# Kernel tuning notes

Hardware: AMD Instinct MI355X
Metric: run time of the kernel (lower is better)

Reference implementation:

```python
import jax, jax.numpy as jnp
import numpy as np

N_NODES = 100000
N_EDGES = 1600000
D_IN, D_H, D_OUT = 512, 128, 64
BN_EPS = 1e-5


def setup_inputs() -> dict:
    key = jax.random.key(0)
    ks = jax.random.split(key, 8)
    x = jax.random.normal(ks[0], (N_NODES, D_IN), dtype=jnp.float32)
    # COO sparse normalized adjacency
    row = jnp.sort(jax.random.randint(ks[1], (N_EDGES,), 0, N_NODES))
    col = jax.random.randint(ks[2], (N_EDGES,), 0, N_NODES)
    adj_vals = jax.random.uniform(ks[3], (N_EDGES,), dtype=jnp.float32) / 16.0
    # GraphConvolution params (xavier_uniform weight, zero bias)
    lim0 = float(np.sqrt(6.0 / (D_IN + D_H)))
    lim1 = float(np.sqrt(6.0 / (D_H + D_OUT)))
    W0 = jax.random.uniform(ks[4], (D_IN, D_H), minval=-lim0, maxval=lim0, dtype=jnp.float32)
    W1 = jax.random.uniform(ks[5], (D_H, D_OUT), minval=-lim1, maxval=lim1, dtype=jnp.float32)
    b0 = jnp.zeros((D_H,), dtype=jnp.float32)
    b1 = jnp.zeros((D_OUT,), dtype=jnp.float32)
    return {"x": x, "W0": W0, "b0": b0, "W1": W1, "b1": b1,
            "adj_vals": adj_vals, "row": row, "col": col}


def _spmm(vals, row, col, h, n):
    # (sparse adj) @ h : gather source rows, scale by edge value, scatter-add to dest
    return jax.ops.segment_sum(vals[:, None] * h[col], row, num_segments=n)


def reference(x, W0, b0, W1, b1, adj_vals, row, col):
    n = x.shape[0]
    # layer 0: adj @ (x @ W0) + b0  (dropout is identity in eval mode)
    h = _spmm(adj_vals, row, col, x @ W0, n) + b0
    h = jax.nn.relu(h)
    # BatchNorm1d(affine=False, track_running_stats=False): batch stats, biased var
    mean = jnp.mean(h, axis=0)
    var = jnp.mean(jnp.square(h - mean), axis=0)
    h = (h - mean) * jax.lax.rsqrt(var + BN_EPS)
    # layer 1: adj @ (h @ W1) + b1
    return _spmm(adj_vals, row, col, h @ W1, n) + b1
```

## Files before the change

### kernel.cpp

```cpp
#include <hip/hip_runtime.h>
#include <hip/hip_bf16.h>
#include <cstdint>
#include <cstddef>

#define D_IN  512
#define D_H   128
#define D_OUT 64
#define SB    256

typedef __attribute__((ext_vector_type(8))) short bf16x8;
typedef __attribute__((ext_vector_type(4))) float f32x4;

__device__ __forceinline__ float bf2f(unsigned short u) {
  union { unsigned int i; float f; } v; v.i = ((unsigned int)u) << 16; return v.f;
}
__device__ __forceinline__ unsigned short f2bf(float f) {
  union { unsigned int i; float f; } v; v.f = f;
  unsigned int r = v.i + 0x7FFFu + ((v.i >> 16) & 1u);
  return (unsigned short)(r >> 16);
}
__device__ __forceinline__ unsigned int pk_bf16(float a, float b) {
  union { __hip_bfloat162 h; unsigned int u; } cv;
  cv.h = __float22bfloat162_rn(make_float2(a, b));
  return cv.u;
}

#define OFF_RP    0u
#define OFF_W0T   400384u
#define OFF_W1TP  531456u
#define OFF_CVEC  547840u
#define OFF_PSUM  548096u
#define OFF_PSQ   679168u
#define OFF_H     810240u
#define END_H     26410240u
#define END_HW    39210240u

__global__ void k_init(const int* __restrict__ row, int* __restrict__ rp,
                       const float* __restrict__ W0, unsigned short* __restrict__ W0t,
                       int n, int e, int RB) {
  int b = blockIdx.x, t = threadIdx.x;
  if (b < RB) {
    int i = b * 256 + t;
    if (i > n) return;
    int lo = 0, hi = e;
    while (lo < hi) { int mid = (lo + hi) >> 1; if (row[mid] < i) lo = mid + 1; else hi = mid; }
    rp[i] = lo;
  } else {
    int idx = (b - RB) * 256 + t;
    int k = idx & (D_IN - 1);
    int nn = idx >> 9;
    W0t[nn * D_IN + k] = f2bf(W0[k * D_H + nn]);
  }
}

__global__ __launch_bounds__(256) void k_gemm1(const float* __restrict__ A,
                                               const unsigned short* __restrict__ Bt,
                                               unsigned short* __restrict__ C, int M) {
  __shared__ unsigned short Ash[2][4096];
  __shared__ unsigned short Bsh[2][4096];
  const int tid = threadIdx.x, lane = tid & 63, wave = tid >> 6;
  const int wm = (wave >> 1) * 64, wn = (wave & 1) * 64;
  const int m0 = blockIdx.x * 128, quad = lane >> 4, l16 = lane & 15;
  f32x4 acc[4][4] = {};
  int am[2], ak[2];
  const float* aptr[2];
  const unsigned short* bptr[2];
#pragma unroll
  for (int i = 0; i < 2; ++i) {
    int c = tid + i * 256;
    am[i] = c >> 2; ak[i] = c & 3;
    int gm = m0 + am[i]; if (gm >= M) gm = M - 1;
    aptr[i] = A + (size_t)gm * D_IN + ak[i] * 8;
    bptr[i] = Bt + (size_t)am[i] * D_IN + ak[i] * 8;
  }
  f32x4 areg[2][2]; bf16x8 breg[2];
#pragma unroll
  for (int i = 0; i < 2; ++i) {
    areg[i][0] = *(const f32x4*)(aptr[i]);
    areg[i][1] = *(const f32x4*)(aptr[i] + 4);
    breg[i]    = *(const bf16x8*)(bptr[i]);
  }
  const int NIT = D_IN / 32;
  for (int it = 0; it < NIT; ++it) {
    const int buf = it & 1;
    unsigned short* ash = Ash[buf];
    unsigned short* bsh = Bsh[buf];
#pragma unroll
    for (int i = 0; i < 2; ++i) {
      unsigned int pk4[4];
      pk4[0] = pk_bf16(areg[i][0][0], areg[i][0][1]);
      pk4[1] = pk_bf16(areg[i][0][2], areg[i][0][3]);
      pk4[2] = pk_bf16(areg[i][1][0], areg[i][1][1]);
      pk4[3] = pk_bf16(areg[i][1][2], areg[i][1][3]);
      *(uint4*)&ash[(ak[i] * 128 + am[i]) * 8] = *(uint4*)pk4;
      *(bf16x8*)&bsh[(ak[i] * 128 + am[i]) * 8] = breg[i];
    }
    __syncthreads();
    if (it + 1 < NIT) {
      int k0 = (it + 1) * 32;
#pragma unroll
      for (int i = 0; i < 2; ++i) {
        areg[i][0] = *(const f32x4*)(aptr[i] + k0);
        areg[i][1] = *(const f32x4*)(aptr[i] + k0 + 4);
        breg[i]    = *(const bf16x8*)(bptr[i] + k0);
      }
    }
    bf16x8 af[4], bfv[4];
#pragma unroll
    for (int mf = 0; mf < 4; ++mf)
      af[mf] = *(const bf16x8*)&ash[(quad * 128 + (wm + mf * 16 + l16)) * 8];
#pragma unroll
    for (int nf = 0; nf < 4; ++nf)
      bfv[nf] = *(const bf16x8*)&bsh[(quad * 128 + (wn + nf * 16 + l16)) * 8];
#pragma unroll
    for (int mf = 0; mf < 4; ++mf)
#pragma unroll
      for (int nf = 0; nf < 4; ++nf)
        acc[mf][nf] = __builtin_amdgcn_mfma_f32_16x16x32_bf16(af[mf], bfv[nf], acc[mf][nf], 0, 0, 0);
  }
#pragma unroll
  for (int mf = 0; mf < 4; ++mf)
#pragma unroll
    for (int nf = 0; nf < 4; ++nf)
#pragma unroll
      for (int i = 0; i < 4; ++i) {
        int r = m0 + wm + mf * 16 + quad * 4 + i;
        int cc = wn + nf * 16 + l16;
        if (r < M) C[(size_t)r * D_H + cc] = f2bf(acc[mf][nf][i]);
      }
}

#define ACCP(P, W) { \
  union { unsigned int u; float f; } _t; \
  _t.u = (P).x << 16;         a0 += (W) * _t.f; \
  _t.u = (P).x & 0xFFFF0000u; a1 += (W) * _t.f; \
  _t.u = (P).y << 16;         a2 += (W) * _t.f; \
  _t.u = (P).y & 0xFFFF0000u; a3 += (W) * _t.f; \
  _t.u = (P).z << 16;         a4 += (W) * _t.f; \
  _t.u = (P).z & 0xFFFF0000u; a5 += (W) * _t.f; \
  _t.u = (P).w << 16;         a6 += (W) * _t.f; \
  _t.u = (P).w & 0xFFFF0000u; a7 += (W) * _t.f; }

__global__ __launch_bounds__(256) void k_spmm1(const unsigned int* __restrict__ xw2,
                                               const float* __restrict__ adj,
                                               const int* __restrict__ col,
                                               const int* __restrict__ rp,
                                               const float* __restrict__ b0,
                                               unsigned int* __restrict__ h2, int n) {
  int node = blockIdx.x * 4 + (threadIdx.x >> 6);
  if (node >= n) return;
  const int l = threadIdx.x & 63;
  const int q = l >> 4, s = l & 15;
  const int e0 = rp[node], e1 = rp[node + 1];
  float a0 = 0.f, a1 = 0.f, a2 = 0.f, a3 = 0.f;
  float a4 = 0.f, a5 = 0.f, a6 = 0.f, a7 = 0.f;
  int e = e0;
  for (; e + 16 <= e1; e += 16) {
    int eb = e + 4 * q;
    int   c0 = col[eb],     c1 = col[eb + 1], c2 = col[eb + 2], c3 = col[eb + 3];
    float w0 = adj[eb],     w1 = adj[eb + 1], w2 = adj[eb + 2], w3 = adj[eb + 3];
    uint4 p0 = *(const uint4*)(xw2 + (size_t)c0 * 64 + 4 * s);
    uint4 p1 = *(const uint4*)(xw2 + (size_t)c1 * 64 + 4 * s);
    uint4 p2 = *(const uint4*)(xw2 + (size_t)c2 * 64 + 4 * s);
    uint4 p3 = *(const uint4*)(xw2 + (size_t)c3 * 64 + 4 * s);
    ACCP(p0, w0); ACCP(p1, w1); ACCP(p2, w2); ACCP(p3, w3);
  }
  for (; e < e1; e += 4) {
    int idx = e + q;
    int ic = idx < e1 ? idx : e1 - 1;
    int   c = col[ic];
    float w = idx < e1 ? adj[ic] : 0.f;
    uint4 p = *(const uint4*)(xw2 + (size_t)c * 64 + 4 * s);
    ACCP(p, w);
  }
#define RED2(v) { v += __shfl_xor(v, 16, 64); v += __shfl_xor(v, 32, 64); }
  RED2(a0) RED2(a1) RED2(a2) RED2(a3) RED2(a4) RED2(a5) RED2(a6) RED2(a7)
#undef RED2
  if (q == 0) {
    float4 bl = *(const float4*)(b0 + 8 * s);
    float4 bh = *(const float4*)(b0 + 8 * s + 4);
    float r0 = fmaxf(a0 + bl.x, 0.f), r1 = fmaxf(a1 + bl.y, 0.f);
    float r2 = fmaxf(a2 + bl.z, 0.f), r3 = fmaxf(a3 + bl.w, 0.f);
    float r4 = fmaxf(a4 + bh.x, 0.f), r5 = fmaxf(a5 + bh.y, 0.f);
    float r6 = fmaxf(a6 + bh.z, 0.f), r7 = fmaxf(a7 + bh.w, 0.f);
    uint4 o;
    o.x = ((unsigned int)f2bf(r1) << 16) | (unsigned int)f2bf(r0);
    o.y = ((unsigned int)f2bf(r3) << 16) | (unsigned int)f2bf(r2);
    o.z = ((unsigned int)f2bf(r5) << 16) | (unsigned int)f2bf(r4);
    o.w = ((unsigned int)f2bf(r7) << 16) | (unsigned int)f2bf(r6);
    *(uint4*)(h2 + (size_t)node * 64 + 4 * s) = o;
  }
}

__global__ __launch_bounds__(256) void k_stats(const unsigned int* __restrict__ h2,
                                               float* __restrict__ psum,
                                               float* __restrict__ psq, int n) {
  __shared__ float sA[256], sB[256], qA[256], qB[256];
  int t = threadIdx.x;
  int f2 = t & 63, rg = t >> 6;
  float s0 = 0.f, s1 = 0.f, q0 = 0.f, q1 = 0.f;
  for (int r = blockIdx.x * 4 + rg; r < n; r += gridDim.x * 4) {
    unsigned int p = h2[(size_t)r * 64 + f2];
    float v0 = bf2f((unsigned short)(p & 0xFFFF));
    float v1 = bf2f((unsigned short)(p >> 16));
    s0 += v0; s1 += v1; q0 += v0 * v0; q1 += v1 * v1;
  }
  sA[t] = s0; sB[t] = s1; qA[t] = q0; qB[t] = q1;
  __syncthreads();
  if (t < 64) {
    float S0 = sA[t] + sA[t + 64] + sA[t + 128] + sA[t + 192];
    float S1 = sB[t] + sB[t + 64] + sB[t + 128] + sB[t + 192];
    float Q0 = qA[t] + qA[t + 64] + qA[t + 128] + qA[t + 192];
    float Q1 = qB[t] + qB[t + 64] + qB[t + 128] + qB[t + 192];
    psum[blockIdx.x * 128 + 2 * t]     = S0;
    psum[blockIdx.x * 128 + 2 * t + 1] = S1;
    psq [blockIdx.x * 128 + 2 * t]     = Q0;
    psq [blockIdx.x * 128 + 2 * t + 1] = Q1;
  }
}

__global__ void k_prep2(const float* __restrict__ psum, const float* __restrict__ psq,
                        const float* __restrict__ W1,
                        unsigned short* __restrict__ W1tp, float* __restrict__ cvec, int n) {
  __shared__ float rs[256], rq[256];
  __shared__ float mean_s[128], istd_s[128];
  __shared__ float cpart[256];
  int t = threadIdx.x;
  int f = t & 127, half = t >> 7;
  {
    float s = 0.f, q = 0.f;
#pragma unroll 8
    for (int b = half * (SB / 2); b < (half + 1) * (SB / 2); ++b) {
      s += psum[b * 128 + f]; q += psq[b * 128 + f];
    }
    rs[t] = s; rq[t] = q;
  }
  __syncthreads();
  if (t < 128) {
    float s = rs[t] + rs[t + 128];
    float q = rq[t] + rq[t + 128];
    float m = s / (float)n;
    float var = q / (float)n - m * m;
    if (var < 0.f) var = 0.f;
    mean_s[t] = m;
    istd_s[t] = rsqrtf(var + 1e-5f);
  }
  __syncthreads();
  for (int idx = t; idx < D_OUT * D_H; idx += 256) {
    int nn = idx >> 7, k = idx & 127;
    W1tp[nn * D_H + k] = f2bf(istd_s[k] * W1[k * D_OUT + nn]);
  }
  {
    int o = t & 63, part = t >> 6;
    float a = 0.f;
    for (int k = part * 32; k < part * 32 + 32; ++k)
      a += mean_s[k] * istd_s[k] * W1[k * D_OUT + o];
    cpart[t] = a;
  }
  __syncthreads();
  if (t < D_OUT)
    cvec[t] = -(cpart[t] + cpart[t + 64] + cpart[t + 128] + cpart[t + 192]);
}

__global__ __launch_bounds__(256) void k_gemm2(const unsigned short* __restrict__ A,
                                               const unsigned short* __restrict__ Bt,
                                               const float* __restrict__ cvec,
                                               unsigned short* __restrict__ Cout, int M) {
  __shared__ unsigned short Ash[4096];
  __shared__ unsigned short Bsh[2048];
  const int tid = threadIdx.x, lane = tid & 63, wave = tid >> 6;
  const int wm = wave * 32, m0 = blockIdx.x * 128;
  const int quad = lane >> 4, l16 = lane & 15;
  f32x4 acc[2][4] = {};
  for (int k0 = 0; k0 < D_H; k0 += 32) {
    __syncthreads();
#pragma unroll
    for (int i = 0; i < 2; ++i) {
      int c = tid + i * 256;
      int m = c >> 2, k8 = c & 3;
      int gm = m0 + m; if (gm >= M) gm = M - 1;
      *(bf16x8*)&Ash[(k8 * 128 + m) * 8] = *(const bf16x8*)&A[(size_t)gm * D_H + k0 + k8 * 8];
    }
    {
      int nn = tid >> 2, k8 = tid & 3;
      *(bf16x8*)&Bsh[(k8 * 64 + nn) * 8] = *(const bf16x8*)&Bt[(size_t)nn * D_H + k0 + k8 * 8];
    }
    __syncthreads();
    bf16x8 af[2], bfv[4];
#pragma unroll
    for (int mf = 0; mf < 2; ++mf)
      af[mf] = *(const bf16x8*)&Ash[(quad * 128 + (wm + mf * 16 + l16)) * 8];
#pragma unroll
    for (int nf = 0; nf < 4; ++nf)
      bfv[nf] = *(const bf16x8*)&Bsh[(quad * 64 + (nf * 16 + l16)) * 8];
#pragma unroll
    for (int mf = 0; mf < 2; ++mf)
#pragma unroll
      for (int nf = 0; nf < 4; ++nf)
        acc[mf][nf] = __builtin_amdgcn_mfma_f32_16x16x32_bf16(af[mf], bfv[nf], acc[mf][nf], 0, 0, 0);
  }
#pragma unroll
  for (int mf = 0; mf < 2; ++mf)
#pragma unroll
    for (int nf = 0; nf < 4; ++nf)
#pragma unroll
      for (int i = 0; i < 4; ++i) {
        int r = m0 + wm + mf * 16 + quad * 4 + i;
        int cc = nf * 16 + l16;
        if (r < M) Cout[(size_t)r * 64 + cc] = f2bf(acc[mf][nf][i] + cvec[cc]);
      }
}

__global__ __launch_bounds__(256) void k_spmm2(const unsigned int* __restrict__ hw2,
                                               const float* __restrict__ adj,
                                               const int* __restrict__ col,
                                               const int* __restrict__ rp,
                                               const float* __restrict__ b1,
                                               float* __restrict__ outp, int n) {
  int node = blockIdx.x * 4 + (threadIdx.x >> 6);
  if (node >= n) return;
  const int l = threadIdx.x & 63;
  const int g = l >> 3, s = l & 7;
  const int e0 = rp[node], e1 = rp[node + 1];
  float a0 = 0.f, a1 = 0.f, a2 = 0.f, a3 = 0.f;
  float a4 = 0.f, a5 = 0.f, a6 = 0.f, a7 = 0.f;
  int e = e0;
  for (; e + 16 <= e1; e += 16) {
    int eb = e + 2 * g;
    int   c0 = col[eb],  c1 = col[eb + 1];
    float w0 = adj[eb],  w1 = adj[eb + 1];
    uint4 p0 = *(const uint4*)(hw2 + (size_t)c0 * 32 + 4 * s);
    uint4 p1 = *(const uint4*)(hw2 + (size_t)c1 * 32 + 4 * s);
    ACCP(p0, w0); ACCP(p1, w1);
  }
  for (; e < e1; e += 8) {
    int idx = e + g;
    int ic = idx < e1 ? idx : e1 - 1;
    int   c = col[ic];
    float w = idx < e1 ? adj[ic] : 0.f;
    uint4 p = *(const uint4*)(hw2 + (size_t)c * 32 + 4 * s);
    ACCP(p, w);
  }
#define RED3(v) { v += __shfl_xor(v, 8, 64); v += __shfl_xor(v, 16, 64); v += __shfl_xor(v, 32, 64); }
  RED3(a0) RED3(a1) RED3(a2) RED3(a3) RED3(a4) RED3(a5) RED3(a6) RED3(a7)
#undef RED3
  if (g == 0) {
    float4 bl = *(const float4*)(b1 + 8 * s);
    float4 bh = *(const float4*)(b1 + 8 * s + 4);
    float4 r0, r1;
    r0.x = a0 + bl.x; r0.y = a1 + bl.y; r0.z = a2 + bl.z; r0.w = a3 + bl.w;
    r1.x = a4 + bh.x; r1.y = a5 + bh.y; r1.z = a6 + bh.z; r1.w = a7 + bh.w;
    *(float4*)(outp + (size_t)node * 64 + 8 * s)     = r0;
    *(float4*)(outp + (size_t)node * 64 + 8 * s + 4) = r1;
  }
}

extern "C" void kernel_launch(void* const* d_in, const int* in_sizes, int n_in,
                              void* d_out, int out_size, void* d_ws, size_t ws_size,
                              hipStream_t stream) {
  const float* x   = (const float*)d_in[0];
  const float* W0  = (const float*)d_in[1];
  const float* b0  = (const float*)d_in[2];
  const float* W1  = (const float*)d_in[3];
  const float* b1  = (const float*)d_in[4];
  const float* adj = (const float*)d_in[5];
  const int* row = (const int*)d_in[6];
  const int* col = (const int*)d_in[7];
  const int N = in_sizes[0] / D_IN;
  const int E = in_sizes[5];

  char* ws = (char*)d_ws;
  int*            rp   = (int*)(ws + OFF_RP);
  unsigned short* W0t  = (unsigned short*)(ws + OFF_W0T);
  unsigned short* W1tp = (unsigned short*)(ws + OFF_W1TP);
  float*          cvec = (float*)(ws + OFF_CVEC);
  float*          psum = (float*)(ws + OFF_PSUM);
  float*          psq  = (float*)(ws + OFF_PSQ);
  unsigned short* h    = (unsigned short*)(ws + OFF_H);

  unsigned short* xw = (unsigned short*)d_out;
  const bool hw_in_ws = (ws_size >= (size_t)END_HW);
  unsigned short* hwp  = hw_in_ws ? (unsigned short*)(ws + END_H) : (unsigned short*)d_out;
  float*          outd = hw_in_ws ? (float*)d_out                 : (float*)(ws + OFF_H);

  const int RB = (N + 1 + 255) / 256;
  const int TB = (D_IN * D_H) / 256;
  k_init<<<RB + TB, 256, 0, stream>>>(row, rp, W0, W0t, N, E, RB);
  k_gemm1<<<(N + 127) / 128, 256, 0, stream>>>(x, W0t, xw, N);
  k_spmm1<<<(N + 3) / 4, 256, 0, stream>>>((const unsigned int*)xw, adj, col, rp, b0,
                                           (unsigned int*)h, N);
  k_stats<<<SB, 256, 0, stream>>>((const unsigned int*)h, psum, psq, N);
  k_prep2<<<1, 256, 0, stream>>>(psum, psq, W1, W1tp, cvec, N);
  k_gemm2<<<(N + 127) / 128, 256, 0, stream>>>(h, W1tp, cvec, hwp, N);
  k_spmm2<<<(N + 3) / 4, 256, 0, stream>>>((const unsigned int*)hwp, adj, col, rp, b1,
                                           outd, N);
  if (!hw_in_ws) {
    hipMemcpyAsync(d_out, outd, (size_t)N * D_OUT * sizeof(float),
                   hipMemcpyDeviceToDevice, stream);
  }
}
```

Measured before the change: 491.9 us.

## Fuse batch-norm statistics into first SpMM via atomic partial sums

The separate statistics kernel, which re-read the whole hidden activation buffer, is removed. Each SpMM1 block now reduces its four rows' sums and squared sums in shared memory and atomically adds them into one of 64 zero-initialised slots. The slots are cleared by an extra block in the init kernel. The intermediate XW buffer moves into the workspace when it is large enough, and the device-to-device copy fallback is dropped. The trade is extra global atomics with contention on 64 slots against one fewer full pass over memory and one fewer launch. Statistics are now taken from fp32 values rather than bf16-rounded ones.

New measurement: 465.6 us. -5.4%, faster.

```diff
diff --git a/kernel.cpp b/kernel.cpp
--- a/kernel.cpp
+++ b/kernel.cpp
@@ -6,7 +6,7 @@
 #define D_IN  512
 #define D_H   128
 #define D_OUT 64
-#define SB    256
+#define SB    64
 
 typedef __attribute__((ext_vector_type(8))) short bf16x8;
 typedef __attribute__((ext_vector_type(4))) float f32x4;
@@ -34,10 +34,13 @@
 #define OFF_H     810240u
 #define END_H     26410240u
 #define END_HW    39210240u
+#define OFF_XW    39210240u
+#define END_XW    64810240u
 
 __global__ void k_init(const int* __restrict__ row, int* __restrict__ rp,
                        const float* __restrict__ W0, unsigned short* __restrict__ W0t,
-                       int n, int e, int RB) {
+                       float* __restrict__ psum, float* __restrict__ psq,
+                       int n, int e, int RB, int TB) {
   int b = blockIdx.x, t = threadIdx.x;
   if (b < RB) {
     int i = b * 256 + t;
@@ -45,11 +48,13 @@
     int lo = 0, hi = e;
     while (lo < hi) { int mid = (lo + hi) >> 1; if (row[mid] < i) lo = mid + 1; else hi = mid; }
     rp[i] = lo;
-  } else {
+  } else if (b < RB + TB) {
     int idx = (b - RB) * 256 + t;
     int k = idx & (D_IN - 1);
     int nn = idx >> 9;
     W0t[nn * D_IN + k] = f2bf(W0[k * D_H + nn]);
+  } else {
+    for (int i = t; i < SB * 128; i += 256) { psum[i] = 0.f; psq[i] = 0.f; }
   }
 }
 
@@ -146,76 +151,70 @@
                                                const int* __restrict__ col,
                                                const int* __restrict__ rp,
                                                const float* __restrict__ b0,
-                                               unsigned int* __restrict__ h2, int n) {
-  int node = blockIdx.x * 4 + (threadIdx.x >> 6);
-  if (node >= n) return;
-  const int l = threadIdx.x & 63;
-  const int q = l >> 4, s = l & 15;
-  const int e0 = rp[node], e1 = rp[node + 1];
-  float a0 = 0.f, a1 = 0.f, a2 = 0.f, a3 = 0.f;
-  float a4 = 0.f, a5 = 0.f, a6 = 0.f, a7 = 0.f;
-  int e = e0;
-  for (; e + 16 <= e1; e += 16) {
-    int eb = e + 4 * q;
-    int   c0 = col[eb],     c1 = col[eb + 1], c2 = col[eb + 2], c3 = col[eb + 3];
-    float w0 = adj[eb],     w1 = adj[eb + 1], w2 = adj[eb + 2], w3 = adj[eb + 3];
-    uint4 p0 = *(const uint4*)(xw2 + (size_t)c0 * 64 + 4 * s);
-    uint4 p1 = *(const uint4*)(xw2 + (size_t)c1 * 64 + 4 * s);
-    uint4 p2 = *(const uint4*)(xw2 + (size_t)c2 * 64 + 4 * s);
-    uint4 p3 = *(const uint4*)(xw2 + (size_t)c3 * 64 + 4 * s);
-    ACCP(p0, w0); ACCP(p1, w1); ACCP(p2, w2); ACCP(p3, w3);
-  }
-  for (; e < e1; e += 4) {
-    int idx = e + q;
-    int ic = idx < e1 ? idx : e1 - 1;
-    int   c = col[ic];
-    float w = idx < e1 ? adj[ic] : 0.f;
-    uint4 p = *(const uint4*)(xw2 + (size_t)c * 64 + 4 * s);
-    ACCP(p, w);
-  }
-#define RED2(v) { v += __shfl_xor(v, 16, 64); v += __shfl_xor(v, 32, 64); }
-  RED2(a0) RED2(a1) RED2(a2) RED2(a3) RED2(a4) RED2(a5) RED2(a6) RED2(a7)
-#undef RED2
-  if (q == 0) {
-    float4 bl = *(const float4*)(b0 + 8 * s);
-    float4 bh = *(const float4*)(b0 + 8 * s + 4);
-    float r0 = fmaxf(a0 + bl.x, 0.f), r1 = fmaxf(a1 + bl.y, 0.f);
-    float r2 = fmaxf(a2 + bl.z, 0.f), r3 = fmaxf(a3 + bl.w, 0.f);
-    float r4 = fmaxf(a4 + bh.x, 0.f), r5 = fmaxf(a5 + bh.y, 0.f);
-    float r6 = fmaxf(a6 + bh.z, 0.f), r7 = fmaxf(a7 + bh.w, 0.f);
-    uint4 o;
-    o.x = ((unsigned int)f2bf(r1) << 16) | (unsigned int)f2bf(r0);
-    o.y = ((unsigned int)f2bf(r3) << 16) | (unsigned int)f2bf(r2);
-    o.z = ((unsigned int)f2bf(r5) << 16) | (unsigned int)f2bf(r4);
-    o.w = ((unsigned int)f2bf(r7) << 16) | (unsigned int)f2bf(r6);
-    *(uint4*)(h2 + (size_t)node * 64 + 4 * s) = o;
-  }
-}
-
-__global__ __launch_bounds__(256) void k_stats(const unsigned int* __restrict__ h2,
+                                               unsigned int* __restrict__ h2,
                                                float* __restrict__ psum,
                                                float* __restrict__ psq, int n) {
-  __shared__ float sA[256], sB[256], qA[256], qB[256];
-  int t = threadIdx.x;
-  int f2 = t & 63, rg = t >> 6;
-  float s0 = 0.f, s1 = 0.f, q0 = 0.f, q1 = 0.f;
-  for (int r = blockIdx.x * 4 + rg; r < n; r += gridDim.x * 4) {
-    unsigned int p = h2[(size_t)r * 64 + f2];
-    float v0 = bf2f((unsigned short)(p & 0xFFFF));
-    float v1 = bf2f((unsigned short)(p >> 16));
-    s0 += v0; s1 += v1; q0 += v0 * v0; q1 += v1 * v1;
-  }
-  sA[t] = s0; sB[t] = s1; qA[t] = q0; qB[t] = q1;
+  __shared__ float sst[512], sqt[512];
+  const int t = threadIdx.x;
+  const int wave = t >> 6, l = t & 63;
+  sst[wave * 128 + l] = 0.f; sst[wave * 128 + 64 + l] = 0.f;
+  sqt[wave * 128 + l] = 0.f; sqt[wave * 128 + 64 + l] = 0.f;
+  const int node = blockIdx.x * 4 + wave;
+  const int q = l >> 4, s = l & 15;
+  if (node < n) {
+    const int e0 = rp[node], e1 = rp[node + 1];
+    float a0 = 0.f, a1 = 0.f, a2 = 0.f, a3 = 0.f;
+    float a4 = 0.f, a5 = 0.f, a6 = 0.f, a7 = 0.f;
+    int e = e0;
+    for (; e + 16 <= e1; e += 16) {
+      int eb = e + 4 * q;
+      int   c0 = col[eb],     c1 = col[eb + 1], c2 = col[eb + 2], c3 = col[eb + 3];
+      float w0 = adj[eb],     w1 = adj[eb + 1], w2 = adj[eb + 2], w3 = adj[eb + 3];
+      uint4 p0 = *(const uint4*)(xw2 + (size_t)c0 * 64 + 4 * s);
+      uint4 p1 = *(const uint4*)(xw2 + (size_t)c1 * 64 + 4 * s);
+      uint4 p2 = *(const uint4*)(xw2 + (size_t)c2 * 64 + 4 * s);
+      uint4 p3 = *(const uint4*)(xw2 + (size_t)c3 * 64 + 4 * s);
+      ACCP(p0, w0); ACCP(p1, w1); ACCP(p2, w2); ACCP(p3, w3);
+    }
+    for (; e < e1; e += 4) {
+      int idx = e + q;
+      int ic = idx < e1 ? idx : e1 - 1;
+      int   c = col[ic];
+      float w = idx < e1 ? adj[ic] : 0.f;
+      uint4 p = *(const uint4*)(xw2 + (size_t)c * 64 + 4 * s);
+      ACCP(p, w);
+    }
+#define RED2(v) { v += __shfl_xor(v, 16, 64); v += __shfl_xor(v, 32, 64); }
+    RED2(a0) RED2(a1) RED2(a2) RED2(a3) RED2(a4) RED2(a5) RED2(a6) RED2(a7)
+#undef RED2
+    if (q == 0) {
+      float4 bl = *(const float4*)(b0 + 8 * s);
+      float4 bh = *(const float4*)(b0 + 8 * s + 4);
+      float r0 = fmaxf(a0 + bl.x, 0.f), r1 = fmaxf(a1 + bl.y, 0.f);
+      float r2 = fmaxf(a2 + bl.z, 0.f), r3 = fmaxf(a3 + bl.w, 0.f);
+      float r4 = fmaxf(a4 + bh.x, 0.f), r5 = fmaxf(a5 + bh.y, 0.f);
+      float r6 = fmaxf(a6 + bh.z, 0.f), r7 = fmaxf(a7 + bh.w, 0.f);
+      uint4 o;
+      o.x = ((unsigned int)f2bf(r1) << 16) | (unsigned int)f2bf(r0);
+      o.y = ((unsigned int)f2bf(r3) << 16) | (unsigned int)f2bf(r2);
+      o.z = ((unsigned int)f2bf(r5) << 16) | (unsigned int)f2bf(r4);
+      o.w = ((unsigned int)f2bf(r7) << 16) | (unsigned int)f2bf(r6);
+      *(uint4*)(h2 + (size_t)node * 64 + 4 * s) = o;
+      float* sw = sst + wave * 128 + 8 * s;
+      float* qw = sqt + wave * 128 + 8 * s;
+      sw[0] = r0; sw[1] = r1; sw[2] = r2; sw[3] = r3;
+      sw[4] = r4; sw[5] = r5; sw[6] = r6; sw[7] = r7;
+      qw[0] = r0 * r0; qw[1] = r1 * r1; qw[2] = r2 * r2; qw[3] = r3 * r3;
+      qw[4] = r4 * r4; qw[5] = r5 * r5; qw[6] = r6 * r6; qw[7] = r7 * r7;
+    }
+  }
   __syncthreads();
-  if (t < 64) {
-    float S0 = sA[t] + sA[t + 64] + sA[t + 128] + sA[t + 192];
-    float S1 = sB[t] + sB[t + 64] + sB[t + 128] + sB[t + 192];
-    float Q0 = qA[t] + qA[t + 64] + qA[t + 128] + qA[t + 192];
-    float Q1 = qB[t] + qB[t + 64] + qB[t + 128] + qB[t + 192];
-    psum[blockIdx.x * 128 + 2 * t]     = S0;
-    psum[blockIdx.x * 128 + 2 * t + 1] = S1;
-    psq [blockIdx.x * 128 + 2 * t]     = Q0;
-    psq [blockIdx.x * 128 + 2 * t + 1] = Q1;
+  if (t < 128) {
+    float S = sst[t] + sst[128 + t] + sst[256 + t] + sst[384 + t];
+    float Q = sqt[t] + sqt[128 + t] + sqt[256 + t] + sqt[384 + t];
+    int slot = (blockIdx.x & (SB - 1)) * 128 + t;
+    atomicAdd(&psum[slot], S);
+    atomicAdd(&psq[slot], Q);
   }
 }
 
@@ -378,24 +377,19 @@
   float*          psq  = (float*)(ws + OFF_PSQ);
   unsigned short* h    = (unsigned short*)(ws + OFF_H);
 
-  unsigned short* xw = (unsigned short*)d_out;
-  const bool hw_in_ws = (ws_size >= (size_t)END_HW);
-  unsigned short* hwp  = hw_in_ws ? (unsigned short*)(ws + END_H) : (unsigned short*)d_out;
-  float*          outd = hw_in_ws ? (float*)d_out                 : (float*)(ws + OFF_H);
+  const bool big_ws = (ws_size >= (size_t)END_XW);
+  unsigned short* xw   = big_ws ? (unsigned short*)(ws + OFF_XW) : (unsigned short*)d_out;
+  unsigned short* hwp  = big_ws ? (unsigned short*)(ws + END_H)  : (unsigned short*)d_out;
+  float*          outd = (float*)d_out;
 
   const int RB = (N + 1 + 255) / 256;
   const int TB = (D_IN * D_H) / 256;
-  k_init<<<RB + TB, 256, 0, stream>>>(row, rp, W0, W0t, N, E, RB);
+  k_init<<<RB + TB + 1, 256, 0, stream>>>(row, rp, W0, W0t, psum, psq, N, E, RB, TB);
   k_gemm1<<<(N + 127) / 128, 256, 0, stream>>>(x, W0t, xw, N);
   k_spmm1<<<(N + 3) / 4, 256, 0, stream>>>((const unsigned int*)xw, adj, col, rp, b0,
-                                           (unsigned int*)h, N);
-  k_stats<<<SB, 256, 0, stream>>>((const unsigned int*)h, psum, psq, N);
+                                           (unsigned int*)h, psum, psq, N);
   k_prep2<<<1, 256, 0, stream>>>(psum, psq, W1, W1tp, cvec, N);
   k_gemm2<<<(N + 127) / 128, 256, 0, stream>>>(h, W1tp, cvec, hwp, N);
   k_spmm2<<<(N + 3) / 4, 256, 0, stream>>>((const unsigned int*)hwp, adj, col, rp, b1,
                                            outd, N);
-  if (!hw_in_ws) {
-    hipMemcpyAsync(d_out, outd, (size_t)N * D_OUT * sizeof(float),
-                   hipMemcpyDeviceToDevice, stream);
-  }
-}
+}
```
